# Optimization experiments

Hardware: AMD Instinct MI355X
Metric: run time of the kernel (lower is better)

## Reference

```python
import jax, jax.numpy as jnp
import numpy as np

B, M, N, D, W = 4, 4096, 4096, 128, 128  # batch/heads, rows, cols, head dim, nnz per row


def setup_inputs() -> dict:
    key = jax.random.key(0)
    kq, kk, kv, kc = jax.random.split(key, 4)
    q3d = jax.random.normal(kq, (B, M, D), dtype=jnp.float32)
    k3d = jax.random.normal(kk, (B, N, D), dtype=jnp.float32)
    v3d = jax.random.normal(kv, (B, N, D), dtype=jnp.float32)
    # CSR with uniform W nonzeros per row: row_offsets = arange(M+1)*W implicitly
    column_indices = jnp.sort(
        jax.random.randint(kc, (M, W), 0, N), axis=-1
    ).astype(jnp.int32)
    return {"q3d": q3d, "k3d": k3d, "v3d": v3d, "column_indices": column_indices}


def reference(q3d, k3d, v3d, column_indices):
    # SDDMM: logits[b, i, j] = q[b, i, :] . k[b, col[i, j], :]  (no 1/sqrt(d) scaling,
    # matching the original module which applies none)
    k_gath = k3d[:, column_indices, :]                     # [B, M, W, D]
    logits = jnp.einsum('bmd,bmwd->bmw', q3d, k_gath)      # [B, M, W]
    # Sparse row-wise softmax over the nonzeros of each row
    weights = jax.nn.softmax(logits, axis=-1)              # [B, M, W]
    # SPMM: out[b, i, :] = sum_j weights[b, i, j] * v[b, col[i, j], :]
    v_gath = v3d[:, column_indices, :]                     # [B, M, W, D]
    out = jnp.einsum('bmw,bmwd->bmd', weights, v_gath)     # [B, M, D]
    return out
```

## Files before the change

kernel.cpp:

```cpp
#include <hip/hip_runtime.h>


typedef __attribute__((ext_vector_type(2))) _Float16 half2v;
typedef __attribute__((ext_vector_type(8))) _Float16 half8;

constexpr int Bc = 4, Mc = 4096, Nc = 4096, Dc = 128, Wc = 128;
constexpr size_t KV_ELEMS = (size_t)Bc * Nc * Dc;
constexpr float EPS_SCREEN = 3e-6f;
constexpr float QS = 127.f / 6.f;
constexpr float INV_S = 1.f / (QS * QS);

__global__ __launch_bounds__(256) void cvt_kernel(
    const float* __restrict__ k3d, _Float16* __restrict__ kh,
    unsigned int* __restrict__ ki8)
{
    const size_t i = ((size_t)blockIdx.x * blockDim.x + threadIdx.x) * 8;
    if (i >= KV_ELEMS) return;
    const float4 ka = *reinterpret_cast<const float4*>(k3d + i);
    const float4 kb = *reinterpret_cast<const float4*>(k3d + i + 4);
    half8 hk;
    hk[0]=(_Float16)ka.x; hk[1]=(_Float16)ka.y; hk[2]=(_Float16)ka.z; hk[3]=(_Float16)ka.w;
    hk[4]=(_Float16)kb.x; hk[5]=(_Float16)kb.y; hk[6]=(_Float16)kb.z; hk[7]=(_Float16)kb.w;
    *reinterpret_cast<half8*>(kh + i) = hk;
    float f[8] = {ka.x, ka.y, ka.z, ka.w, kb.x, kb.y, kb.z, kb.w};
    unsigned int w0 = 0, w1 = 0;
    #pragma unroll
    for (int jj = 0; jj < 4; ++jj) {
        int v = __float2int_rn(f[jj] * QS);
        v = max(-127, min(127, v));
        w0 |= ((unsigned int)(v & 0xFF)) << (8 * jj);
    }
    #pragma unroll
    for (int jj = 0; jj < 4; ++jj) {
        int v = __float2int_rn(f[4 + jj] * QS);
        v = max(-127, min(127, v));
        w1 |= ((unsigned int)(v & 0xFF)) << (8 * jj);
    }
    *reinterpret_cast<uint2*>(ki8 + i / 4) = make_uint2(w0, w1);
}

__device__ __forceinline__ float dot8_f16(const half8& qv, const half8& kv) {
    const half2v q0 = {qv[0], qv[1]}, q1 = {qv[2], qv[3]},
                 q2 = {qv[4], qv[5]}, q3 = {qv[6], qv[7]};
    const half2v k0 = {kv[0], kv[1]}, k1 = {kv[2], kv[3]},
                 k2 = {kv[4], kv[5]}, k3 = {kv[6], kv[7]};
    float p = __builtin_amdgcn_fdot2(q0, k0, 0.f, false);
    p = __builtin_amdgcn_fdot2(q1, k1, p, false);
    p = __builtin_amdgcn_fdot2(q2, k2, p, false);
    p = __builtin_amdgcn_fdot2(q3, k3, p, false);
    return p;
}

__global__ __launch_bounds__(64) void sparse_attn_r13(
    const float*        __restrict__ q3d,
    const _Float16*     __restrict__ kh,
    const unsigned int* __restrict__ ki8,
    const float*        __restrict__ v3d,
    const int*          __restrict__ cidx,
    float*              __restrict__ out)
{
    const int blk = blockIdx.x;
    const int xcd = blk & 7;
    const int b   = xcd >> 1;
    const int m   = ((blk >> 3) << 1) | (xcd & 1);
    const int j   = threadIdx.x;

    __shared__ __align__(16) _Float16 qsh[Dc];
    __shared__ __align__(16) unsigned int qpk[Dc / 4];
    __shared__ int   cs[Wc];
    __shared__ int   part[8][Wc + 4];
    __shared__ float rpart[16][17];
    __shared__ int   widx[Wc];
    __shared__ float ls2[Wc];
    __shared__ float wp[Wc];

    {
        const size_t qb = ((size_t)b * Mc + m) * Dc;
        const float qf0 = q3d[qb + j];
        const float qf1 = q3d[qb + 64 + j];
        qsh[j]      = (_Float16)qf0;
        qsh[64 + j] = (_Float16)qf1;
        int v0 = __float2int_rn(qf0 * QS); v0 = max(-127, min(127, v0));
        int v1 = __float2int_rn(qf1 * QS); v1 = max(-127, min(127, v1));
        reinterpret_cast<signed char*>(qpk)[j]      = (signed char)v0;
        reinterpret_cast<signed char*>(qpk)[64 + j] = (signed char)v1;
        cs[j]      = cidx[m * Wc + j];
        cs[64 + j] = cidx[m * Wc + 64 + j];
        widx[j] = 0; widx[64 + j] = 0;
        wp[j] = 0.f; wp[64 + j] = 0.f;
    }
    __syncthreads();

    const int c8 = j & 7;
    const int r8 = j >> 3;
    const uint4* kbq = reinterpret_cast<const uint4*>(ki8 + (size_t)b * Nc * Dc / 4);
    const int qd0 = (int)qpk[c8 * 4 + 0], qd1 = (int)qpk[c8 * 4 + 1],
              qd2 = (int)qpk[c8 * 4 + 2], qd3 = (int)qpk[c8 * 4 + 3];

    int rb[16];
    #pragma unroll
    for (int i = 0; i < 16; ++i) rb[i] = cs[i * 8 + r8] * 8 + c8;
    uint4 kr[16];
    #pragma unroll
    for (int i = 0; i < 16; ++i) kr[i] = kbq[rb[i]];
    #pragma unroll
    for (int i = 0; i < 16; ++i) {
        int d = __builtin_amdgcn_sdot4(qd0, (int)kr[i].x, 0, false);
        d = __builtin_amdgcn_sdot4(qd1, (int)kr[i].y, d, false);
        d = __builtin_amdgcn_sdot4(qd2, (int)kr[i].z, d, false);
        d = __builtin_amdgcn_sdot4(qd3, (int)kr[i].w, d, false);
        part[c8][i * 8 + r8] = d;
    }
    __syncthreads();

    int Li0 = 0, Li1 = 0;
    #pragma unroll
    for (int c = 0; c < 8; ++c) { Li0 += part[c][j]; Li1 += part[c][64 + j]; }
    const float L0 = (float)Li0 * INV_S;
    const float L1 = (float)Li1 * INV_S;

    float mx = fmaxf(L0, L1);
    #pragma unroll
    for (int o = 32; o; o >>= 1) mx = fmaxf(mx, __shfl_xor(mx, o));
    const float e0 = __expf(L0 - mx), e1 = __expf(L1 - mx);
    float ssum = e0 + e1;
    #pragma unroll
    for (int o = 32; o; o >>= 1) ssum += __shfl_xor(ssum, o);
    const float inv_ssum = 1.f / ssum;

    const unsigned long long mk0 = __ballot(e0 * inv_ssum >= EPS_SCREEN);
    const unsigned long long mk1 = __ballot(e1 * inv_ssum >= EPS_SCREEN);
    const int n0 = __popcll(mk0);
    const int n  = n0 + __popcll(mk1);
    const unsigned long long lt = (j == 0) ? 0ull : (~0ull >> (64 - j));
    if (mk0 & (1ull << j)) widx[__popcll(mk0 & lt)]      = cs[j];
    if (mk1 & (1ull << j)) widx[n0 + __popcll(mk1 & lt)] = cs[64 + j];
    __syncthreads();

    const int c16 = j & 15;
    const int r4  = j >> 4;
    const half8*  kb16 = reinterpret_cast<const half8*>(kh + (size_t)b * Nc * Dc);
    const float4* vb4  = reinterpret_cast<const float4*>(v3d + (size_t)b * Nc * Dc);
    const half8 qv = *reinterpret_cast<const half8*>(&qsh[c16 * 8]);

    half8 kk[4];
    #pragma unroll
    for (int v = 0; v < 4; ++v) {
        const int slot = v * 4 + r4;
        kk[v] = (slot < n) ? kb16[widx[slot] * 16 + c16] : half8{};
    }
    const int h = j >> 5, c32 = j & 31;
    float4 vr[8];
    #pragma unroll
    for (int i = 0; i < 8; ++i) {
        vr[i] = vb4[(size_t)widx[2 * i + h] * 32 + c32];
    }

    #pragma unroll
    for (int v = 0; v < 4; ++v)
        rpart[v * 4 + r4][c16] = dot8_f16(qv, kk[v]);
    __syncthreads();
    if (j < 16) {
        float sum = 0.f;
        #pragma unroll
        for (int c = 0; c < 16; ++c) sum += rpart[j][c];
        ls2[j] = sum;
    }
    for (int base = 16; base < n; base += 16) {
        __syncthreads();
        #pragma unroll
        for (int v = 0; v < 4; ++v) {
            const int slot = base + v * 4 + r4;
            half8 kx = (slot < n) ? kb16[widx[slot] * 16 + c16] : half8{};
            rpart[v * 4 + r4][c16] = dot8_f16(qv, kx);
        }
        __syncthreads();
        if (j < 16 && base + j < n) {
            float sum = 0.f;
            #pragma unroll
            for (int c = 0; c < 16; ++c) sum += rpart[j][c];
            ls2[base + j] = sum;
        }
    }
    __syncthreads();

    const float A  = (j < n)      ? ls2[j]      : -1e30f;
    const float B2 = (64 + j < n) ? ls2[64 + j] : -1e30f;
    float mx2 = fmaxf(A, B2);
    #pragma unroll
    for (int o = 32; o; o >>= 1) mx2 = fmaxf(mx2, __shfl_xor(mx2, o));
    const float ea = (j < n)      ? __expf(A - mx2)  : 0.f;
    const float eb = (64 + j < n) ? __expf(B2 - mx2) : 0.f;
    float s2 = ea + eb;
    #pragma unroll
    for (int o = 32; o; o >>= 1) s2 += __shfl_xor(s2, o);
    const float i2 = 1.f / s2;
    if (j < n)      wp[j]      = ea * i2;
    if (64 + j < n) wp[64 + j] = eb * i2;
    __syncthreads();

    float4 acc = {0.f, 0.f, 0.f, 0.f};
    #pragma unroll
    for (int i = 0; i < 8; ++i) {
        const float w = wp[2 * i + h];
        acc.x += w * vr[i].x; acc.y += w * vr[i].y;
        acc.z += w * vr[i].z; acc.w += w * vr[i].w;
    }
    for (int slot = 16 + h; slot < n; slot += 2) {
        const float w = wp[slot];
        const float4 v4 = vb4[(size_t)widx[slot] * 32 + c32];
        acc.x += w * v4.x; acc.y += w * v4.y;
        acc.z += w * v4.z; acc.w += w * v4.w;
    }
    acc.x += __shfl_xor(acc.x, 32);
    acc.y += __shfl_xor(acc.y, 32);
    acc.z += __shfl_xor(acc.z, 32);
    acc.w += __shfl_xor(acc.w, 32);
    if (j < 32)
        reinterpret_cast<float4*>(out + ((size_t)b * Mc + m) * Dc)[j] = acc;
}

extern "C" void kernel_launch(void* const* d_in, const int* in_sizes, int n_in,
                              void* d_out, int out_size, void* d_ws, size_t ws_size,
                              hipStream_t stream) {
    const float* q = (const float*)d_in[0];
    const float* k = (const float*)d_in[1];
    const float* v = (const float*)d_in[2];
    const int*   c = (const int*)d_in[3];
    float*       o = (float*)d_out;
    (void)in_sizes; (void)n_in; (void)out_size; (void)ws_size;

    _Float16*     kh  = (_Float16*)d_ws;
    unsigned int* ki8 = (unsigned int*)((char*)d_ws + KV_ELEMS * sizeof(_Float16));

    const int cvt_threads = 256;
    const int cvt_blocks  = (int)(KV_ELEMS / 8 / cvt_threads);
    cvt_kernel<<<cvt_blocks, cvt_threads, 0, stream>>>(k, kh, ki8);

    sparse_attn_r13<<<dim3(Bc * Mc), dim3(64), 0, stream>>>(q, kh, ki8, v, c, o);
}
```

Baseline: 100.0 us.

## Compute int8 screening logits with MFMA 16x16x64 instead of sdot4 plus LDS reduction

Replaces the per-thread sdot4 partial dot products, their shared-memory partial-sum array and the extra barrier with int8 MFMA instructions. The K rows are laid out as MFMA B operands and the query as the A operand, and only row 0 of each accumulator is used as the logit. The softmax max, sum and ballot screening are restructured around the 16-lane MFMA output layout. This removes LDS traffic and a sync, but wastes 15 of 16 MFMA rows and depends on the operand-layout mapping being correct.

```diff
diff --git a/kernel.cpp b/kernel.cpp
--- a/kernel.cpp
+++ b/kernel.cpp
@@ -3,6 +3,7 @@
 
 typedef __attribute__((ext_vector_type(2))) _Float16 half2v;
 typedef __attribute__((ext_vector_type(8))) _Float16 half8;
+typedef __attribute__((ext_vector_type(4))) int i32x4;
 
 constexpr int Bc = 4, Mc = 4096, Nc = 4096, Dc = 128, Wc = 128;
 constexpr size_t KV_ELEMS = (size_t)Bc * Nc * Dc;
@@ -51,7 +52,7 @@
     return p;
 }
 
-__global__ __launch_bounds__(64) void sparse_attn_r13(
+__global__ __launch_bounds__(64) void sparse_attn_r14(
     const float*        __restrict__ q3d,
     const _Float16*     __restrict__ kh,
     const unsigned int* __restrict__ ki8,
@@ -68,7 +69,6 @@
     __shared__ __align__(16) _Float16 qsh[Dc];
     __shared__ __align__(16) unsigned int qpk[Dc / 4];
     __shared__ int   cs[Wc];
-    __shared__ int   part[8][Wc + 4];
     __shared__ float rpart[16][17];
     __shared__ int   widx[Wc];
     __shared__ float ls2[Wc];
@@ -91,45 +91,54 @@
     }
     __syncthreads();
 
-    const int c8 = j & 7;
-    const int r8 = j >> 3;
+    const int n16 = j & 15;
+    const int qd  = j >> 4;
     const uint4* kbq = reinterpret_cast<const uint4*>(ki8 + (size_t)b * Nc * Dc / 4);
-    const int qd0 = (int)qpk[c8 * 4 + 0], qd1 = (int)qpk[c8 * 4 + 1],
-              qd2 = (int)qpk[c8 * 4 + 2], qd3 = (int)qpk[c8 * 4 + 3];
-
-    int rb[16];
-    #pragma unroll
-    for (int i = 0; i < 16; ++i) rb[i] = cs[i * 8 + r8] * 8 + c8;
+
+    int rowb[8];
+    #pragma unroll
+    for (int t = 0; t < 8; ++t) rowb[t] = cs[t * 16 + n16] * 8;
     uint4 kr[16];
     #pragma unroll
-    for (int i = 0; i < 16; ++i) kr[i] = kbq[rb[i]];
-    #pragma unroll
-    for (int i = 0; i < 16; ++i) {
-        int d = __builtin_amdgcn_sdot4(qd0, (int)kr[i].x, 0, false);
-        d = __builtin_amdgcn_sdot4(qd1, (int)kr[i].y, d, false);
-        d = __builtin_amdgcn_sdot4(qd2, (int)kr[i].z, d, false);
-        d = __builtin_amdgcn_sdot4(qd3, (int)kr[i].w, d, false);
-        part[c8][i * 8 + r8] = d;
-    }
-    __syncthreads();
-
-    int Li0 = 0, Li1 = 0;
-    #pragma unroll
-    for (int c = 0; c < 8; ++c) { Li0 += part[c][j]; Li1 += part[c][64 + j]; }
-    const float L0 = (float)Li0 * INV_S;
-    const float L1 = (float)Li1 * INV_S;
-
-    float mx = fmaxf(L0, L1);
-    #pragma unroll
-    for (int o = 32; o; o >>= 1) mx = fmaxf(mx, __shfl_xor(mx, o));
-    const float e0 = __expf(L0 - mx), e1 = __expf(L1 - mx);
-    float ssum = e0 + e1;
-    #pragma unroll
-    for (int o = 32; o; o >>= 1) ssum += __shfl_xor(ssum, o);
+    for (int t = 0; t < 8; ++t) {
+        kr[2 * t]     = kbq[rowb[t] + qd];
+        kr[2 * t + 1] = kbq[rowb[t] + 4 + qd];
+    }
+
+    const i32x4 af0 = *reinterpret_cast<const i32x4*>(&qpk[qd * 4]);
+    const i32x4 af1 = *reinterpret_cast<const i32x4*>(&qpk[16 + qd * 4]);
+
+    i32x4 acc[8];
+    #pragma unroll
+    for (int t = 0; t < 8; ++t) {
+        i32x4 a = {0, 0, 0, 0};
+        a = __builtin_amdgcn_mfma_i32_16x16x64_i8(af0, *reinterpret_cast<i32x4*>(&kr[2 * t]),     a, 0, 0, 0);
+        a = __builtin_amdgcn_mfma_i32_16x16x64_i8(af1, *reinterpret_cast<i32x4*>(&kr[2 * t + 1]), a, 0, 0, 0);
+        acc[t] = a;
+    }
+
+    float Lt[8];
+    #pragma unroll
+    for (int t = 0; t < 8; ++t) Lt[t] = (float)acc[t][0] * INV_S;
+    float mx = Lt[0];
+    #pragma unroll
+    for (int t = 1; t < 8; ++t) mx = fmaxf(mx, Lt[t]);
+    #pragma unroll
+    for (int o = 8; o; o >>= 1) mx = fmaxf(mx, __shfl_xor(mx, o));
+    float et[8], ssum = 0.f;
+    #pragma unroll
+    for (int t = 0; t < 8; ++t) { et[t] = __expf(Lt[t] - mx); ssum += et[t]; }
+    #pragma unroll
+    for (int o = 8; o; o >>= 1) ssum += __shfl_xor(ssum, o);
     const float inv_ssum = 1.f / ssum;
 
-    const unsigned long long mk0 = __ballot(e0 * inv_ssum >= EPS_SCREEN);
-    const unsigned long long mk1 = __ballot(e1 * inv_ssum >= EPS_SCREEN);
+    unsigned long long mk0 = 0ull, mk1 = 0ull;
+    #pragma unroll
+    for (int t = 0; t < 4; ++t)
+        mk0 |= (__ballot(et[t] * inv_ssum >= EPS_SCREEN) & 0xFFFFull) << (16 * t);
+    #pragma unroll
+    for (int t = 4; t < 8; ++t)
+        mk1 |= (__ballot(et[t] * inv_ssum >= EPS_SCREEN) & 0xFFFFull) << (16 * (t - 4));
     const int n0 = __popcll(mk0);
     const int n  = n0 + __popcll(mk1);
     const unsigned long long lt = (j == 0) ? 0ull : (~0ull >> (64 - j));
@@ -199,25 +208,25 @@
     if (64 + j < n) wp[64 + j] = eb * i2;
     __syncthreads();
 
-    float4 acc = {0.f, 0.f, 0.f, 0.f};
+    float4 oacc = {0.f, 0.f, 0.f, 0.f};
     #pragma unroll
     for (int i = 0; i < 8; ++i) {
         const float w = wp[2 * i + h];
-        acc.x += w * vr[i].x; acc.y += w * vr[i].y;
-        acc.z += w * vr[i].z; acc.w += w * vr[i].w;
+        oacc.x += w * vr[i].x; oacc.y += w * vr[i].y;
+        oacc.z += w * vr[i].z; oacc.w += w * vr[i].w;
     }
     for (int slot = 16 + h; slot < n; slot += 2) {
         const float w = wp[slot];
         const float4 v4 = vb4[(size_t)widx[slot] * 32 + c32];
-        acc.x += w * v4.x; acc.y += w * v4.y;
-        acc.z += w * v4.z; acc.w += w * v4.w;
-    }
-    acc.x += __shfl_xor(acc.x, 32);
-    acc.y += __shfl_xor(acc.y, 32);
-    acc.z += __shfl_xor(acc.z, 32);
-    acc.w += __shfl_xor(acc.w, 32);
+        oacc.x += w * v4.x; oacc.y += w * v4.y;
+        oacc.z += w * v4.z; oacc.w += w * v4.w;
+    }
+    oacc.x += __shfl_xor(oacc.x, 32);
+    oacc.y += __shfl_xor(oacc.y, 32);
+    oacc.z += __shfl_xor(oacc.z, 32);
+    oacc.w += __shfl_xor(oacc.w, 32);
     if (j < 32)
-        reinterpret_cast<float4*>(out + ((size_t)b * Mc + m) * Dc)[j] = acc;
+        reinterpret_cast<float4*>(out + ((size_t)b * Mc + m) * Dc)[j] = oacc;
 }
 
 extern "C" void kernel_launch(void* const* d_in, const int* in_sizes, int n_in,
@@ -237,5 +246,5 @@
     const int cvt_blocks  = (int)(KV_ELEMS / 8 / cvt_threads);
     cvt_kernel<<<cvt_blocks, cvt_threads, 0, stream>>>(k, kh, ki8);
 
-    sparse_attn_r13<<<dim3(Bc * Mc), dim3(64), 0, stream>>>(q, kh, ki8, v, c, o);
-}
+    sparse_attn_r14<<<dim3(Bc * Mc), dim3(64), 0, stream>>>(q, kh, ki8, v, c, o);
+}
```

Measured after the change: 113.6 us. +13.6%, slower.
